# Kernel tuning notes

Measured on AMD Instinct MI355X. Metric: run time of the kernel, lower is better.

Reference implementation:

```python
import jax, jax.numpy as jnp
import numpy as np

N_ATOMS = 2_000_000
N_MOL = 100_000
ATOMS_PER_MOL = 20
FEAT_DIM = 128
MAX_Z = 86


def setup_inputs() -> dict:
    key = jax.random.key(0)
    k_z, k_f, k_w, k_b = jax.random.split(key, 4)
    z = jax.random.randint(k_z, (N_ATOMS,), 1, MAX_Z)  # avoid padding_idx 0
    f = jax.random.normal(k_f, (N_ATOMS, FEAT_DIM), dtype=jnp.float32)
    num_atoms = jnp.full((N_MOL,), ATOMS_PER_MOL, dtype=jnp.int64)
    w_e = jax.random.normal(k_w, (FEAT_DIM, 1), dtype=jnp.float32) / np.sqrt(FEAT_DIM)
    z_bias = jax.random.normal(k_b, (MAX_Z, 1), dtype=jnp.float32)
    z_bias = z_bias.at[0].set(0.0)  # padding_idx=0 row is zero
    return {"z": z, "f": f, "num_atoms": num_atoms, "w_e": w_e, "z_bias": z_bias}


def reference(z, f, num_atoms, w_e, z_bias):
    n_total = f.shape[0]
    n_mol = num_atoms.shape[0]
    # atomwise energy: linear(feat->1, no bias) + per-element embedding bias
    atomwise = f @ w_e + z_bias[z]  # [N, 1]
    # segment ids: molecule index for each atom (scatter_mol's index tensor)
    seg = jnp.repeat(jnp.arange(n_mol), num_atoms, total_repeat_length=n_total)
    e_total = jax.ops.segment_sum(atomwise, seg, num_segments=n_mol)  # [B, 1]
    return e_total
```

## Files before the change

### kernel.cpp

```cpp
#include <hip/hip_runtime.h>


#define FEAT 128
#define SCAN_CHUNK 1024
#define SCAN_THREADS 256

__global__ void k_partial_sums(const int* __restrict__ cnt, int n,
                               int* __restrict__ block_sums) {
    __shared__ int sdata[SCAN_THREADS];
    const int chunk_base = blockIdx.x * SCAN_CHUNK;
    int local = 0;
    for (int i = threadIdx.x; i < SCAN_CHUNK; i += SCAN_THREADS) {
        int idx = chunk_base + i;
        if (idx < n) local += cnt[idx];
    }
    sdata[threadIdx.x] = local;
    __syncthreads();
    for (int s = SCAN_THREADS / 2; s > 0; s >>= 1) {
        if (threadIdx.x < s) sdata[threadIdx.x] += sdata[threadIdx.x + s];
        __syncthreads();
    }
    if (threadIdx.x == 0) block_sums[blockIdx.x] = sdata[0];
}

__global__ void k_offsets(const int* __restrict__ cnt, int n,
                          const int* __restrict__ block_sums,
                          int* __restrict__ offsets) {
    __shared__ int tsum[SCAN_THREADS];
    __shared__ int s_prefix;
    const int t = threadIdx.x;

    int p = 0;
    for (int j = t; j < blockIdx.x; j += SCAN_THREADS) p += block_sums[j];
    tsum[t] = p;
    __syncthreads();
    for (int s = SCAN_THREADS / 2; s > 0; s >>= 1) {
        if (t < s) tsum[t] += tsum[t + s];
        __syncthreads();
    }
    if (t == 0) s_prefix = tsum[0];
    __syncthreads();
    const int chunk_prefix = s_prefix;
    __syncthreads();

    const int chunk_base = blockIdx.x * SCAN_CHUNK;
    const int per_thread = SCAN_CHUNK / SCAN_THREADS;
    const int base_idx = chunk_base + t * per_thread;

    int v[per_thread];
    int s = 0;
#pragma unroll
    for (int j = 0; j < per_thread; ++j) {
        int idx = base_idx + j;
        v[j] = (idx < n) ? cnt[idx] : 0;
        s += v[j];
    }
    tsum[t] = s;
    __syncthreads();

    for (int off = 1; off < SCAN_THREADS; off <<= 1) {
        int val = (t >= off) ? tsum[t - off] : 0;
        __syncthreads();
        tsum[t] += val;
        __syncthreads();
    }
    int running = chunk_prefix + (tsum[t] - s);
#pragma unroll
    for (int j = 0; j < per_thread; ++j) {
        int idx = base_idx + j;
        if (idx < n) offsets[idx] = running;
        running += v[j];
    }
}

__global__ void __launch_bounds__(256)
k_readout(const float* __restrict__ f, const int* __restrict__ z,
          const int* __restrict__ cnt, const int* __restrict__ offsets,
          const float* __restrict__ w_e, const float* __restrict__ z_bias,
          float* __restrict__ out, int n_mol) {
    const int lane  = threadIdx.x & 63;
    const int wave  = threadIdx.x >> 6;
    const int m0    = (blockIdx.x * 4 + wave) * 4;
    if (m0 >= n_mol) return;

    const int half  = lane >> 5;
    const int qlane = lane & 31;

    const float4 w = reinterpret_cast<const float4*>(w_e)[qlane];
    const float4* __restrict__ f4 = reinterpret_cast<const float4*>(f);

    bool fast = (m0 + 4 <= n_mol);
    int c0 = 0, c1 = 0, c2 = 0, c3 = 0;
    if (fast) {
        c0 = cnt[m0]; c1 = cnt[m0 + 1]; c2 = cnt[m0 + 2]; c3 = cnt[m0 + 3];
        fast = (c0 == 20) & (c1 == 20) & (c2 == 20) & (c3 == 20);
    }

    if (fast) {
        const int s0 = offsets[m0];
        float acc0 = 0.f, acc1 = 0.f, acc2 = 0.f, acc3 = 0.f;

        {
            float b = z_bias[z[s0 + lane]];
            acc0 += (lane < 20) ? b : 0.f;
            acc1 += (lane >= 20 && lane < 40) ? b : 0.f;
            acc2 += (lane >= 40 && lane < 60) ? b : 0.f;
            acc3 += (lane >= 60) ? b : 0.f;
            if (lane < 16) acc3 += z_bias[z[s0 + 64 + lane]];
        }

        const float4* __restrict__ fr =
            f4 + (size_t)(s0 + half) * (FEAT / 4) + qlane;
#define ACC(p) ((p) < 10 ? acc0 : ((p) < 20 ? acc1 : ((p) < 30 ? acc2 : acc3)))
#pragma unroll
        for (int b = 0; b < 5; ++b) {
            float4 v[8];
#pragma unroll
            for (int q = 0; q < 8; ++q)
                v[q] = fr[(size_t)(b * 8 + q) * (2 * FEAT / 4)];
#pragma unroll
            for (int q = 0; q < 8; ++q) {
                const int p = b * 8 + q;
                float a = ACC(p);
                a = fmaf(v[q].x, w.x, a);
                a = fmaf(v[q].y, w.y, a);
                a = fmaf(v[q].z, w.z, a);
                a = fmaf(v[q].w, w.w, a);
                ACC(p) = a;
            }
        }
#undef ACC

#pragma unroll
        for (int off = 32; off > 0; off >>= 1) {
            acc0 += __shfl_down(acc0, off);
            acc1 += __shfl_down(acc1, off);
            acc2 += __shfl_down(acc2, off);
            acc3 += __shfl_down(acc3, off);
        }
        if (lane == 0)
            *reinterpret_cast<float4*>(out + m0) =
                make_float4(acc0, acc1, acc2, acc3);
    } else {
        for (int k = 0; k < 4 && m0 + k < n_mol; ++k) {
            const int m = m0 + k;
            const int start = offsets[m];
            const int c = cnt[m];
            float acc = 0.f;
            for (int i = lane; i < c; i += 64) acc += z_bias[z[start + i]];
            const int pairs = c >> 1;
            for (int p = 0; p < pairs; ++p) {
                float4 fv = f4[(size_t)(start + 2 * p + half) * (FEAT / 4) + qlane];
                acc = fmaf(fv.x, w.x, acc);
                acc = fmaf(fv.y, w.y, acc);
                acc = fmaf(fv.z, w.z, acc);
                acc = fmaf(fv.w, w.w, acc);
            }
            if ((c & 1) && half == 0) {
                float4 fv = f4[(size_t)(start + c - 1) * (FEAT / 4) + qlane];
                acc = fmaf(fv.x, w.x, acc);
                acc = fmaf(fv.y, w.y, acc);
                acc = fmaf(fv.z, w.z, acc);
                acc = fmaf(fv.w, w.w, acc);
            }
#pragma unroll
            for (int off = 32; off > 0; off >>= 1) acc += __shfl_down(acc, off);
            if (lane == 0) out[m] = acc;
        }
    }
}

extern "C" void kernel_launch(void* const* d_in, const int* in_sizes, int n_in,
                              void* d_out, int out_size, void* d_ws, size_t ws_size,
                              hipStream_t stream) {
    const int*   z      = (const int*)d_in[0];
    const float* f      = (const float*)d_in[1];
    const int*   cnt    = (const int*)d_in[2];
    const float* w_e    = (const float*)d_in[3];
    const float* z_bias = (const float*)d_in[4];
    float* out = (float*)d_out;

    const int n_mol = in_sizes[2];

    int* offsets    = (int*)d_ws;
    const int nb    = (n_mol + SCAN_CHUNK - 1) / SCAN_CHUNK;
    int* block_sums = offsets + n_mol;

    k_partial_sums<<<nb, SCAN_THREADS, 0, stream>>>(cnt, n_mol, block_sums);
    k_offsets<<<nb, SCAN_THREADS, 0, stream>>>(cnt, n_mol, block_sums, offsets);

    const int n_waves = (n_mol + 3) / 4;
    const int grid    = (n_waves + 3) / 4;
    k_readout<<<grid, 256, 0, stream>>>(f, z, cnt, offsets, w_e, z_bias,
                                        out, n_mol);
}
```

Baseline: 180.9 us.

## Replace two-pass offset scan with uniform-count check and nontemporal feature loads

Drops the two-kernel prefix scan over molecule counts. A single kernel now only checks whether every molecule has exactly 20 atoms. When all counts match, the readout computes start offsets as m0*20 directly; otherwise each wave sums all preceding counts itself, which costs O(n) per wave. Feature loads become nontemporal to avoid polluting the cache with streamed data. This removes one launch and the offset array traffic, but every readout block now reads the full flags array, and the fallback path becomes quadratic for non-uniform inputs.

```diff
diff --git a/kernel.cpp b/kernel.cpp
--- a/kernel.cpp
+++ b/kernel.cpp
@@ -2,85 +2,56 @@
 
 
 #define FEAT 128
-#define SCAN_CHUNK 1024
-#define SCAN_THREADS 256
+#define CHECK_CHUNK 1024
+#define CHECK_THREADS 256
+#define UNIFORM_C 20
 
-__global__ void k_partial_sums(const int* __restrict__ cnt, int n,
-                               int* __restrict__ block_sums) {
-    __shared__ int sdata[SCAN_THREADS];
-    const int chunk_base = blockIdx.x * SCAN_CHUNK;
-    int local = 0;
-    for (int i = threadIdx.x; i < SCAN_CHUNK; i += SCAN_THREADS) {
-        int idx = chunk_base + i;
-        if (idx < n) local += cnt[idx];
-    }
-    sdata[threadIdx.x] = local;
-    __syncthreads();
-    for (int s = SCAN_THREADS / 2; s > 0; s >>= 1) {
-        if (threadIdx.x < s) sdata[threadIdx.x] += sdata[threadIdx.x + s];
-        __syncthreads();
-    }
-    if (threadIdx.x == 0) block_sums[blockIdx.x] = sdata[0];
+typedef float f32x4_t __attribute__((ext_vector_type(4)));
+
+__device__ __forceinline__ float4 ldnt(const float4* p) {
+    f32x4_t v = __builtin_nontemporal_load((const f32x4_t*)p);
+    return make_float4(v.x, v.y, v.z, v.w);
 }
 
-__global__ void k_offsets(const int* __restrict__ cnt, int n,
-                          const int* __restrict__ block_sums,
-                          int* __restrict__ offsets) {
-    __shared__ int tsum[SCAN_THREADS];
-    __shared__ int s_prefix;
-    const int t = threadIdx.x;
-
-    int p = 0;
-    for (int j = t; j < blockIdx.x; j += SCAN_THREADS) p += block_sums[j];
-    tsum[t] = p;
+__global__ void k_check_uniform(const int* __restrict__ cnt, int n,
+                                int* __restrict__ flags) {
+    __shared__ int s_w[CHECK_THREADS / 64];
+    const int base = blockIdx.x * CHECK_CHUNK;
+    bool ok = true;
+    for (int i = threadIdx.x; i < CHECK_CHUNK; i += CHECK_THREADS) {
+        int idx = base + i;
+        if (idx < n && cnt[idx] != UNIFORM_C) ok = false;
+    }
+    bool wave_ok = __all(ok);
+    if ((threadIdx.x & 63) == 0) s_w[threadIdx.x >> 6] = wave_ok ? 1 : 0;
     __syncthreads();
-    for (int s = SCAN_THREADS / 2; s > 0; s >>= 1) {
-        if (t < s) tsum[t] += tsum[t + s];
-        __syncthreads();
-    }
-    if (t == 0) s_prefix = tsum[0];
-    __syncthreads();
-    const int chunk_prefix = s_prefix;
-    __syncthreads();
-
-    const int chunk_base = blockIdx.x * SCAN_CHUNK;
-    const int per_thread = SCAN_CHUNK / SCAN_THREADS;
-    const int base_idx = chunk_base + t * per_thread;
-
-    int v[per_thread];
-    int s = 0;
+    if (threadIdx.x == 0) {
+        int fl = 1;
 #pragma unroll
-    for (int j = 0; j < per_thread; ++j) {
-        int idx = base_idx + j;
-        v[j] = (idx < n) ? cnt[idx] : 0;
-        s += v[j];
-    }
-    tsum[t] = s;
-    __syncthreads();
-
-    for (int off = 1; off < SCAN_THREADS; off <<= 1) {
-        int val = (t >= off) ? tsum[t - off] : 0;
-        __syncthreads();
-        tsum[t] += val;
-        __syncthreads();
-    }
-    int running = chunk_prefix + (tsum[t] - s);
-#pragma unroll
-    for (int j = 0; j < per_thread; ++j) {
-        int idx = base_idx + j;
-        if (idx < n) offsets[idx] = running;
-        running += v[j];
+        for (int wv = 0; wv < CHECK_THREADS / 64; ++wv) fl &= s_w[wv];
+        flags[blockIdx.x] = fl;
     }
 }
 
 __global__ void __launch_bounds__(256)
 k_readout(const float* __restrict__ f, const int* __restrict__ z,
-          const int* __restrict__ cnt, const int* __restrict__ offsets,
+          const int* __restrict__ cnt, const int* __restrict__ flags,
+          int n_flags,
           const float* __restrict__ w_e, const float* __restrict__ z_bias,
           float* __restrict__ out, int n_mol) {
-    const int lane  = threadIdx.x & 63;
-    const int wave  = threadIdx.x >> 6;
-    const int m0    = (blockIdx.x * 4 + wave) * 4;
+    __shared__ int s_w[4];
+    const int t = threadIdx.x;
+
+    bool ok = true;
+    for (int j = t; j < n_flags; j += 256) ok &= (flags[j] != 0);
+    bool wave_ok = __all(ok);
+    if ((t & 63) == 0) s_w[t >> 6] = wave_ok ? 1 : 0;
+    __syncthreads();
+    const bool uniform = s_w[0] && s_w[1] && s_w[2] && s_w[3];
+
+    const int lane = t & 63;
+    const int wave = t >> 6;
+    const int m0 = (blockIdx.x * 4 + wave) * 4;
     if (m0 >= n_mol) return;
 
     const int half  = lane >> 5;
@@ -89,15 +60,8 @@
     const float4 w = reinterpret_cast<const float4*>(w_e)[qlane];
     const float4* __restrict__ f4 = reinterpret_cast<const float4*>(f);
 
-    bool fast = (m0 + 4 <= n_mol);
-    int c0 = 0, c1 = 0, c2 = 0, c3 = 0;
-    if (fast) {
-        c0 = cnt[m0]; c1 = cnt[m0 + 1]; c2 = cnt[m0 + 2]; c3 = cnt[m0 + 3];
-        fast = (c0 == 20) & (c1 == 20) & (c2 == 20) & (c3 == 20);
-    }
-
-    if (fast) {
-        const int s0 = offsets[m0];
+    if (uniform && (m0 + 4 <= n_mol)) {
+        const int s0 = m0 * UNIFORM_C;
         float acc0 = 0.f, acc1 = 0.f, acc2 = 0.f, acc3 = 0.f;
 
         {
@@ -117,7 +81,7 @@
             float4 v[8];
 #pragma unroll
             for (int q = 0; q < 8; ++q)
-                v[q] = fr[(size_t)(b * 8 + q) * (2 * FEAT / 4)];
+                v[q] = ldnt(fr + (size_t)(b * 8 + q) * (2 * FEAT / 4));
 #pragma unroll
             for (int q = 0; q < 8; ++q) {
                 const int p = b * 8 + q;
@@ -142,9 +106,15 @@
             *reinterpret_cast<float4*>(out + m0) =
                 make_float4(acc0, acc1, acc2, acc3);
     } else {
+        int partial = 0;
+        for (int j = lane; j < m0; j += 64) partial += cnt[j];
+#pragma unroll
+        for (int off = 32; off > 0; off >>= 1)
+            partial += __shfl_down(partial, off);
+        int start = __shfl(partial, 0);
+
         for (int k = 0; k < 4 && m0 + k < n_mol; ++k) {
             const int m = m0 + k;
-            const int start = offsets[m];
             const int c = cnt[m];
             float acc = 0.f;
             for (int i = lane; i < c; i += 64) acc += z_bias[z[start + i]];
@@ -166,6 +136,7 @@
 #pragma unroll
             for (int off = 32; off > 0; off >>= 1) acc += __shfl_down(acc, off);
             if (lane == 0) out[m] = acc;
+            start += c;
         }
     }
 }
@@ -182,15 +153,13 @@
 
     const int n_mol = in_sizes[2];
 
-    int* offsets    = (int*)d_ws;
-    const int nb    = (n_mol + SCAN_CHUNK - 1) / SCAN_CHUNK;
-    int* block_sums = offsets + n_mol;
+    int* flags = (int*)d_ws;
+    const int nb = (n_mol + CHECK_CHUNK - 1) / CHECK_CHUNK;
 
-    k_partial_sums<<<nb, SCAN_THREADS, 0, stream>>>(cnt, n_mol, block_sums);
-    k_offsets<<<nb, SCAN_THREADS, 0, stream>>>(cnt, n_mol, block_sums, offsets);
+    k_check_uniform<<<nb, CHECK_THREADS, 0, stream>>>(cnt, n_mol, flags);
 
     const int n_waves = (n_mol + 3) / 4;
     const int grid    = (n_waves + 3) / 4;
-    k_readout<<<grid, 256, 0, stream>>>(f, z, cnt, offsets, w_e, z_bias,
-                                        out, n_mol);
+    k_readout<<<grid, 256, 0, stream>>>(f, z, cnt, flags, nb,
+                                        w_e, z_bias, out, n_mol);
 }
```

New measurement: 156.6 us. 1.16x faster.
